# Optimization experiments

Measured on AMD Instinct MI355X. Metric: run time of the kernel, lower is better.

The kernel has to match this reference:

```python
import jax, jax.numpy as jnp
import numpy as np

DIM = 2048
H = 16
DH = DIM // H          # 128 per-head content dim
LATENT = 512
D_ROPE = 64
B, S = 2, 2048
ROPE_THETA = 10000.0


def _rope_cos_sin(seq_len, d_rope, dtype=jnp.float32):
    # [S, d_rope] cos/sin tables, rotate-half convention
    inv_freq = 1.0 / (ROPE_THETA ** (jnp.arange(0, d_rope, 2, dtype=jnp.float32) / d_rope))
    freqs = jnp.arange(seq_len, dtype=jnp.float32)[:, None] * inv_freq[None, :]  # [S, d_rope/2]
    emb = jnp.concatenate([freqs, freqs], axis=-1)  # [S, d_rope]
    return jnp.cos(emb).astype(dtype), jnp.sin(emb).astype(dtype)


def _rotate_half(x):
    x1, x2 = jnp.split(x, 2, axis=-1)
    return jnp.concatenate([-x2, x1], axis=-1)


def _apply_rope(x, cos, sin):
    # x: [..., S, ..., d_rope]; cos/sin broadcastable to x
    return x * cos + _rotate_half(x) * sin


def setup_inputs() -> dict:
    key = jax.random.key(0)
    ks = jax.random.split(key, 6)
    std = 0.02
    return {
        "x": jax.random.normal(ks[0], (B, S, DIM), jnp.float32),
        "Wq": jax.random.normal(ks[1], (DIM, H * (DH + D_ROPE)), jnp.float32) * std,
        "Wdkv": jax.random.normal(ks[2], (DIM, LATENT), jnp.float32) * std,
        "Wkr": jax.random.normal(ks[3], (DIM, D_ROPE), jnp.float32) * std,
        "Wukv": jax.random.normal(ks[4], (LATENT, H * 2 * DH), jnp.float32) * std,
        "Wo": jax.random.normal(ks[5], (H * DH, DIM), jnp.float32) * std,
    }


def reference(x, Wq, Wdkv, Wkr, Wukv, Wo):
    Bd, Sd, _ = x.shape
    # --- queries: per-head content + decoupled rope part ---
    q = (x @ Wq).reshape(Bd, Sd, H, DH + D_ROPE)
    q_nope, q_rope = q[..., :DH], q[..., DH:]            # [B,S,H,DH], [B,S,H,D_ROPE]
    # --- compressed latent KV ---
    c_kv = x @ Wdkv                                      # [B,S,LATENT]
    kv = (c_kv @ Wukv).reshape(Bd, Sd, H, 2 * DH)
    k_nope, v = kv[..., :DH], kv[..., DH:]               # [B,S,H,DH]
    # --- shared (head-agnostic) rotary key ---
    k_rope = x @ Wkr                                     # [B,S,D_ROPE]
    cos, sin = _rope_cos_sin(Sd, D_ROPE, x.dtype)
    q_rope = _apply_rope(q_rope, cos[None, :, None, :], sin[None, :, None, :])
    k_rope = _apply_rope(k_rope, cos[None, :, :], sin[None, :, :])
    # --- attention scores: content + decoupled rope term ---
    scale = 1.0 / jnp.sqrt(jnp.asarray(DH + D_ROPE, x.dtype))
    scores = jnp.einsum("bqhd,bkhd->bhqk", q_nope, k_nope)
    scores = scores + jnp.einsum("bqhd,bkd->bhqk", q_rope, k_rope)
    scores = scores * scale
    causal = jnp.tril(jnp.ones((Sd, Sd), dtype=bool))
    scores = jnp.where(causal[None, None, :, :], scores, jnp.asarray(-1e9, x.dtype))
    attn = jax.nn.softmax(scores, axis=-1)               # [B,H,S,S]
    out = jnp.einsum("bhqk,bkhd->bqhd", attn, v).reshape(Bd, Sd, H * DH)
    return out @ Wo                                      # [B,S,DIM]
```

## Files before the change

### kernel.cpp

```cpp
#include <hip/hip_runtime.h>
#include <hip/hip_bf16.h>

using bf16 = __hip_bfloat16;
typedef __bf16 bf16x8 __attribute__((ext_vector_type(8)));
typedef float f32x4 __attribute__((ext_vector_type(4)));

#define MFMA16(A, B, C) __builtin_amdgcn_mfma_f32_16x16x32_bf16((A), (B), (C), 0, 0, 0)

__device__ __forceinline__ void store_elem(bf16* p, float v) { *p = __float2bfloat16(v); }
__device__ __forceinline__ void store_elem(float* p, float v) { *p = v; }

__device__ __forceinline__ unsigned short f2bu(float x) {
    bf16 t = __float2bfloat16(x);
    return *(unsigned short*)&t;
}

__device__ __forceinline__ void async_cp16(const bf16* g, bf16* l) {
    __builtin_amdgcn_global_load_lds(
        (const __attribute__((address_space(1))) void*)g,
        (__attribute__((address_space(3))) void*)l, 16, 0, 0);
}

__global__ void cvt_fp32_bf16(const float* __restrict__ src, bf16* __restrict__ dst) {
    int i = (blockIdx.x * 256 + threadIdx.x) * 4;
    float4 v = *(const float4*)(src + i);
    bf16 o[4] = {__float2bfloat16(v.x), __float2bfloat16(v.y),
                 __float2bfloat16(v.z), __float2bfloat16(v.w)};
    *(uint2*)(dst + i) = *(const uint2*)o;
}

__global__ void wtrans(const float* __restrict__ src, bf16* __restrict__ dst,
                       int K, int N) {
    __shared__ bf16 t[32][33];
    int n0 = blockIdx.x * 32, k0 = blockIdx.y * 32;
    #pragma unroll
    for (int i = 0; i < 4; ++i) {
        int r = threadIdx.y + i * 8;
        t[r][threadIdx.x] = __float2bfloat16(src[(size_t)(k0 + r) * N + n0 + threadIdx.x]);
    }
    __syncthreads();
    #pragma unroll
    for (int i = 0; i < 4; ++i) {
        int r = threadIdx.y + i * 8;
        dst[(size_t)(n0 + r) * K + k0 + threadIdx.x] = t[threadIdx.x][r];
    }
}

__global__ void zerofill(bf16* __restrict__ p) {
    p[blockIdx.x * 256 + threadIdx.x] = __float2bfloat16(0.0f);
}

template <typename CT>
__global__ __launch_bounds__(256) void gemm_bt(
    const bf16* __restrict__ A, int lda,
    const bf16* __restrict__ Bt, int ldb,
    CT* __restrict__ C, int ldc, int K) {
    __shared__ bf16 As[2][128 * 32];
    __shared__ bf16 Bs[2][128 * 32];
    const int nwg = gridDim.x * gridDim.y;
    const int flat = blockIdx.y * gridDim.x + blockIdx.x;
    const int swz = (flat & 7) * (nwg >> 3) + (flat >> 3);
    const int m0 = (swz / gridDim.x) * 128;
    const int n0 = (swz % gridDim.x) * 128;
    const int tid = threadIdx.x;
    const int lane = tid & 63;
    const int wave = tid >> 6;
    const int wm = (wave >> 1) * 64;
    const int wn = (wave & 1) * 64;
    const int lr = lane & 15;
    const int lq = lane >> 4;
    const int sr = tid >> 2;
    const int sc = (tid & 3) * 8;
    const int wbase = wave * 512;

    f32x4 acc[4][4] = {};

#define G_STAGE(BUF, KO) do {                                                  \
        async_cp16(A + (size_t)(m0 + sr) * lda + (KO) + sc, As[BUF] + wbase);  \
        async_cp16(A + (size_t)(m0 + sr + 64) * lda + (KO) + sc,               \
                   As[BUF] + 2048 + wbase);                                    \
        async_cp16(Bt + (size_t)(n0 + sr) * ldb + (KO) + sc, Bs[BUF] + wbase); \
        async_cp16(Bt + (size_t)(n0 + sr + 64) * ldb + (KO) + sc,              \
                   Bs[BUF] + 2048 + wbase);                                    \
    } while (0)

    G_STAGE(0, 0);
    __syncthreads();
    int cur = 0;
    for (int k0 = 0; k0 < K; k0 += 32) {
        if (k0 + 32 < K) G_STAGE(cur ^ 1, k0 + 32);
        bf16x8 af[4], bfr[4];
        #pragma unroll
        for (int t = 0; t < 4; ++t) {
            af[t]  = *(const bf16x8*)(As[cur] + (wm + t * 16 + lr) * 32 + lq * 8);
            bfr[t] = *(const bf16x8*)(Bs[cur] + (wn + t * 16 + lr) * 32 + lq * 8);
        }
        #pragma unroll
        for (int mt = 0; mt < 4; ++mt)
            #pragma unroll
            for (int nt = 0; nt < 4; ++nt)
                acc[mt][nt] = MFMA16(af[mt], bfr[nt], acc[mt][nt]);
        __syncthreads();
        cur ^= 1;
    }
#undef G_STAGE
    #pragma unroll
    for (int mt = 0; mt < 4; ++mt)
        #pragma unroll
        for (int nt = 0; nt < 4; ++nt)
            #pragma unroll
            for (int r = 0; r < 4; ++r) {
                int row = m0 + wm + mt * 16 + lq * 4 + r;
                int col = n0 + wn + nt * 16 + lr;
                store_elem(C + (size_t)row * ldc + col, acc[mt][nt][r]);
            }
}

__global__ __launch_bounds__(256) void gemm_kv(
    const bf16* __restrict__ A, int lda,
    const bf16* __restrict__ Bt, int ldb,
    bf16* __restrict__ kbuf, bf16* __restrict__ vT, int K) {
    __shared__ bf16 As[2][128 * 32];
    __shared__ bf16 Bs[2][128 * 32];
    const int nwg = gridDim.x * gridDim.y;
    const int flat = blockIdx.y * gridDim.x + blockIdx.x;
    const int swz = (flat & 7) * (nwg >> 3) + (flat >> 3);
    const int m0 = (swz / gridDim.x) * 128;
    const int n0 = (swz % gridDim.x) * 128;
    const int tid = threadIdx.x;
    const int lane = tid & 63;
    const int wave = tid >> 6;
    const int wm = (wave >> 1) * 64;
    const int wn = (wave & 1) * 64;
    const int lr = lane & 15;
    const int lq = lane >> 4;
    const int sr = tid >> 2;
    const int sc = (tid & 3) * 8;
    const int wbase = wave * 512;

    f32x4 acc[4][4] = {};

#define G_STAGE(BUF, KO) do {                                                  \
        async_cp16(A + (size_t)(m0 + sr) * lda + (KO) + sc, As[BUF] + wbase);  \
        async_cp16(A + (size_t)(m0 + sr + 64) * lda + (KO) + sc,               \
                   As[BUF] + 2048 + wbase);                                    \
        async_cp16(Bt + (size_t)(n0 + sr) * ldb + (KO) + sc, Bs[BUF] + wbase); \
        async_cp16(Bt + (size_t)(n0 + sr + 64) * ldb + (KO) + sc,              \
                   Bs[BUF] + 2048 + wbase);                                    \
    } while (0)

    G_STAGE(0, 0);
    __syncthreads();
    int cur = 0;
    for (int k0 = 0; k0 < K; k0 += 32) {
        if (k0 + 32 < K) G_STAGE(cur ^ 1, k0 + 32);
        bf16x8 af[4], bfr[4];
        #pragma unroll
        for (int t = 0; t < 4; ++t) {
            af[t]  = *(const bf16x8*)(As[cur] + (wm + t * 16 + lr) * 32 + lq * 8);
            bfr[t] = *(const bf16x8*)(Bs[cur] + (wn + t * 16 + lr) * 32 + lq * 8);
        }
        #pragma unroll
        for (int mt = 0; mt < 4; ++mt)
            #pragma unroll
            for (int nt = 0; nt < 4; ++nt)
                acc[mt][nt] = MFMA16(af[mt], bfr[nt], acc[mt][nt]);
        __syncthreads();
        cur ^= 1;
    }
#undef G_STAGE
    #pragma unroll
    for (int mt = 0; mt < 4; ++mt)
        #pragma unroll
        for (int nt = 0; nt < 4; ++nt) {
            int colbase = n0 + wn + nt * 16;
            int h = colbase >> 8;
            int rr = (colbase & 255) + lr;
            #pragma unroll
            for (int r = 0; r < 4; ++r) {
                int row = m0 + wm + mt * 16 + lq * 4 + r;
                bf16 val = __float2bfloat16(acc[mt][nt][r]);
                if (rr < 128) {
                    kbuf[(size_t)row * 2048 + h * 128 + rr] = val;
                } else {
                    int dv = rr - 128;
                    int b = row >> 11, s = row & 2047;
                    vT[((size_t)((b * 16 + h) * 128 + dv)) * 2048 + s] = val;
                }
            }
        }
}

__global__ void rope_kernel(bf16* __restrict__ XW) {
    int v = blockIdx.x;
    int row = blockIdx.y * 4 + threadIdx.y;
    int i = threadIdx.x;
    int s = row & 2047;
    int cbase = (v < 16) ? v * 192 + 128 : 3072;
    size_t base = (size_t)row * 3712 + cbase;
    float xi = __bfloat162float(XW[base + i]);
    float xp = __shfl_xor(xi, 32);
    int j = i & 31;
    float inv = exp2f(-(float)j * (13.287712379549449f / 32.0f));
    float ang = (float)s * inv;
    float c = cosf(ang), sn = sinf(ang);
    float res = (i < 32) ? (xi * c - xp * sn) : (xi * c + xp * sn);
    XW[base + i] = __float2bfloat16(res);
}

__global__ __launch_bounds__(256, 2) void attn_kernel(
    const bf16* __restrict__ XW, const bf16* __restrict__ kbuf,
    const bf16* __restrict__ vT, bf16* __restrict__ attn_out,
    bf16* __restrict__ opart, float* __restrict__ mlbuf) {
    const int bid = blockIdx.x;
    const int half = bid >> 8;
    const int rem = bid & 255;
    const int bh = rem & 31;
    const int p = rem >> 5;
    const int b = bh >> 4, h = bh & 15;
    const int tid = threadIdx.x;
    const int wave = tid >> 6;
    const int lane = tid & 63;
    const int lr = lane & 15, lq = lane >> 4;

    __shared__ bf16 Ks[2][64 * 128];
    __shared__ bf16 Vs[128 * 64];
    __shared__ bf16 Pm[4 * 32 * 72];
    bf16* Pw = Pm + wave * (32 * 72);

    const bf16* xwb = XW + (size_t)b * 2048 * 3712;
    const bf16* kb  = kbuf + (size_t)b * 2048 * 2048 + h * 128;
    const bf16* rp  = xwb + 3072;
    const bf16* vTb = vT + (size_t)bh * 128 * 2048;

    const float sc2 = 0.07216878364870323f * 1.4426950408889634f;

    const int s_rsub = lane >> 4;
    const int s_j    = lane & 15;
#define STAGE_K(N0, BUF) do {                                                  \
        _Pragma("unroll")                                                      \
        for (int k_ = 0; k_ < 4; ++k_) {                                       \
            int i_ = wave * 4 + k_;                                            \
            int r_ = i_ * 4 + s_rsub;                                          \
            int j_ = s_j ^ (r_ & 7);                                           \
            async_cp16(kb + (size_t)((N0) + r_) * 2048 + j_ * 8,               \
                       (BUF) + i_ * 512);                                      \
        }                                                                      \
    } while (0)

#define STAGE_V(N0) do {                                                       \
        _Pragma("unroll")                                                      \
        for (int k_ = 0; k_ < 4; ++k_) {                                       \
            int i_ = wave * 4 + k_;                                            \
            int r_ = i_ * 8 + (lane >> 3);                                     \
            int j_ = (lane & 7) ^ (r_ & 7);                                    \
            async_cp16(vTb + (size_t)r_ * 2048 + (N0) + j_ * 8,                \
                       Vs + i_ * 512);                                         \
        }                                                                      \
    } while (0)

    const int rs = lr & 7;
    int koff[4];
    #pragma unroll
    for (int c = 0; c < 4; ++c) koff[c] = ((c * 4 + lq) ^ rs) * 8;
    int voff[2];
    voff[0] = (lq ^ rs) * 8;
    voff[1] = ((4 + lq) ^ rs) * 8;

    #pragma unroll 1
    for (int ph = 0; ph < 2; ++ph) {
        const int u = ph ? (15 - p) : p;
        const int qw = u * 128 + wave * 32;
        const int hnt = u + 1;
        const int t0 = half ? hnt : 0;
        const int t1 = half ? (2 * u + 2) : hnt;

        bf16x8 qf[2][6];
        #pragma unroll
        for (int nf = 0; nf < 2; ++nf) {
            size_t ro = (size_t)(qw + nf * 16 + lr) * 3712 + h * 192;
            #pragma unroll
            for (int c = 0; c < 6; ++c)
                qf[nf][c] = *(const bf16x8*)(xwb + ro + c * 32 + lq * 8);
        }

        f32x4 o[2][8] = {};
        float m_i[2], l_i[2];
        m_i[0] = m_i[1] = -1e30f;
        l_i[0] = l_i[1] = 0.0f;

        STAGE_K(t0 * 64, Ks[0]);
        int par = 0;

        for (int t = t0; t < t1; ++t) {
            const int n0 = t * 64;
            __syncthreads();

            bf16x8 rf[2][4];
            #pragma unroll
            for (int c = 0; c < 2; ++c)
                #pragma unroll
                for (int mt = 0; mt < 4; ++mt)
                    rf[c][mt] = *(const bf16x8*)(rp + (size_t)(n0 + mt * 16 + lr) * 3712 + c * 32 + lq * 8);

            STAGE_V(n0);
            if (t + 1 < t1) STAGE_K((t + 1) * 64, Ks[par ^ 1]);

            if (n0 < qw + 32) {
                const bf16* Kc = Ks[par];
                f32x4 st[4][2] = {};
                __builtin_amdgcn_s_setprio(1);
                #pragma unroll
                for (int c = 0; c < 4; ++c) {
                    #pragma unroll
                    for (int mt = 0; mt < 4; ++mt) {
                        bf16x8 kf = *(const bf16x8*)(Kc + (mt * 16 + lr) * 128 + koff[c]);
                        st[mt][0] = MFMA16(kf, qf[0][c], st[mt][0]);
                        st[mt][1] = MFMA16(kf, qf[1][c], st[mt][1]);
                    }
                }
                #pragma unroll
                for (int c = 0; c < 2; ++c) {
                    #pragma unroll
                    for (int mt = 0; mt < 4; ++mt) {
                        st[mt][0] = MFMA16(rf[c][mt], qf[0][c + 4], st[mt][0]);
                        st[mt][1] = MFMA16(rf[c][mt], qf[1][c + 4], st[mt][1]);
                    }
                }
                __builtin_amdgcn_s_setprio(0);

                #pragma unroll
                for (int nf = 0; nf < 2; ++nf) {
                    int q = qw + nf * 16 + lr;
                    f32x4 a[4];
                    #pragma unroll
                    for (int mt = 0; mt < 4; ++mt) a[mt] = st[mt][nf];
                    if (n0 + 63 > qw + nf * 16) {
                        #pragma unroll
                        for (int mt = 0; mt < 4; ++mt)
                            #pragma unroll
                            for (int r = 0; r < 4; ++r) {
                                int kid = n0 + mt * 16 + lq * 4 + r;
                                if (kid > q) a[mt][r] = -1e30f;
                            }
                    }
                    f32x4 m4 = a[0];
                    #pragma unroll
                    for (int mt = 1; mt < 4; ++mt)
                        #pragma unroll
                        for (int r = 0; r < 4; ++r) m4[r] = fmaxf(m4[r], a[mt][r]);
                    float vm = fmaxf(fmaxf(m4[0], m4[1]), fmaxf(m4[2], m4[3]));
                    vm = fmaxf(vm, __shfl_xor(vm, 16));
                    vm = fmaxf(vm, __shfl_xor(vm, 32));
                    vm *= sc2;
                    if (__any(vm > m_i[nf] + 8.0f)) {
                        float mnew = fmaxf(m_i[nf], vm);
                        float alpha = exp2f(m_i[nf] - mnew);
                        m_i[nf] = mnew;
                        l_i[nf] *= alpha;
                        #pragma unroll
                        for (int dt = 0; dt < 8; ++dt)
                            #pragma unroll
                            for (int r = 0; r < 4; ++r) o[nf][dt][r] *= alpha;
                    }
                    float mi = m_i[nf];
                    float ps = 0.0f;
                    #pragma unroll
                    for (int mt = 0; mt < 4; ++mt) {
                        unsigned short pk[4];
                        #pragma unroll
                        for (int r = 0; r < 4; ++r) {
                            float pv = exp2f(fmaf(a[mt][r], sc2, -mi));
                            ps += pv;
                            pk[r] = f2bu(pv);
                        }
                        *(uint2*)((unsigned short*)Pw + (nf * 16 + lr) * 72 + mt * 16 + lq * 4) =
                            *(uint2*)pk;
                    }
                    ps += __shfl_xor(ps, 16);
                    ps += __shfl_xor(ps, 32);
                    l_i[nf] += ps;
                }
            }

            __syncthreads();

            if (n0 < qw + 32) {
                bf16x8 ptf[2][2];
                #pragma unroll
                for (int nf = 0; nf < 2; ++nf)
                    #pragma unroll
                    for (int kt = 0; kt < 2; ++kt)
                        ptf[nf][kt] = *(const bf16x8*)(Pw + (nf * 16 + lr) * 72 + kt * 32 + lq * 8);
                __builtin_amdgcn_s_setprio(1);
                #pragma unroll
                for (int kt = 0; kt < 2; ++kt)
                    #pragma unroll
                    for (int dt = 0; dt < 8; ++dt) {
                        bf16x8 vfr = *(const bf16x8*)(Vs + (dt * 16 + lr) * 64 + voff[kt]);
                        o[0][dt] = MFMA16(vfr, ptf[0][kt], o[0][dt]);
                        o[1][dt] = MFMA16(vfr, ptf[1][kt], o[1][dt]);
                    }
                __builtin_amdgcn_s_setprio(0);
            }
            par ^= 1;
        }

        #pragma unroll
        for (int nf = 0; nf < 2; ++nf) {
            float l = l_i[nf];
            float wsc = (l > 0.0f) ? (1.0f / l) : 0.0f;
            float sst = (l > 0.0f) ? (m_i[nf] + log2f(l)) : -1e30f;
            __asm__ volatile("s_waitcnt lgkmcnt(0)" ::: "memory");
            #pragma unroll
            for (int dt = 0; dt < 8; ++dt) {
                unsigned short pk[4];
                #pragma unroll
                for (int r = 0; r < 4; ++r) pk[r] = f2bu(o[nf][dt][r] * wsc);
                *(uint2*)((unsigned short*)Pw + lr * 136 + dt * 16 + lq * 4) = *(uint2*)pk;
            }
            __asm__ volatile("s_waitcnt lgkmcnt(0)" ::: "memory");
            int ql = lane >> 2, cs = (lane & 3) * 32;
            int qrow = qw + nf * 16 + ql;
            uint4 d[4];
            #pragma unroll
            for (int k = 0; k < 4; ++k)
                d[k] = *(const uint4*)(Pw + ql * 136 + cs + k * 8);
            bf16* dst = (half ? opart : attn_out) +
                        (size_t)(b * 2048 + qrow) * 2048 + h * 128 + cs;
            #pragma unroll
            for (int k = 0; k < 4; ++k) *(uint4*)(dst + k * 8) = d[k];
            if (lane < 16) {
                int q2 = qw + nf * 16 + lane;
                mlbuf[((size_t)(b * 2048 + q2) * 16 + h) * 2 + half] = sst;
            }
        }
    }
#undef STAGE_K
#undef STAGE_V
}

__global__ void attn_merge(const bf16* __restrict__ opart,
                           const float* __restrict__ mlbuf,
                           bf16* __restrict__ attn_out) {
    int bs = blockIdx.x;
    int h = blockIdx.y * 2 + threadIdx.y;
    int tx = threadIdx.x;
    const float* mlp = mlbuf + ((size_t)bs * 16 + h) * 2;
    float s0 = mlp[0], s1 = mlp[1];
    size_t off = (size_t)bs * 2048 + h * 128 + tx;
    float o0 = __bfloat162float(attn_out[off]);
    float o1 = __bfloat162float(opart[off]);
    float m = fmaxf(s0, s1);
    float w0 = exp2f(s0 - m);
    float w1 = exp2f(s1 - m);
    float v = (o0 * w0 + o1 * w1) / (w0 + w1);
    attn_out[off] = __float2bfloat16(v);
}

extern "C" void kernel_launch(void* const* d_in, const int* in_sizes, int n_in,
                              void* d_out, int out_size, void* d_ws, size_t ws_size,
                              hipStream_t stream) {
    const float* x    = (const float*)d_in[0];
    const float* Wq   = (const float*)d_in[1];
    const float* Wdkv = (const float*)d_in[2];
    const float* Wkr  = (const float*)d_in[3];
    const float* Wukv = (const float*)d_in[4];
    const float* Wo   = (const float*)d_in[5];
    float* out = (float*)d_out;

    char* ws = (char*)d_ws;
    bf16* XW       = (bf16*)(ws);
    bf16* kbuf     = (bf16*)(ws + 30408704);
    bf16* vT       = (bf16*)(ws + 47185920);
    bf16* attn_out = (bf16*)(ws + 63963136);
    bf16* opart    = (bf16*)(ws + 80740352);
    float* mlbuf   = (float*)(ws + 97517568);
    bf16* xb       = (bf16*)(ws + 30408704);
    bf16* WcatT    = (bf16*)(ws + 47185920);
    bf16* WukvT    = (bf16*)(ws + 63963136);
    bf16* WoT      = (bf16*)(ws + 47185920);

    dim3 tb(32, 8);
    cvt_fp32_bf16<<<8192, 256, 0, stream>>>(x, xb);
    wtrans<<<dim3(96, 64), tb, 0, stream>>>(Wq, WcatT, 2048, 3072);
    wtrans<<<dim3(2, 64), tb, 0, stream>>>(Wkr, WcatT + (size_t)3072 * 2048, 2048, 64);
    wtrans<<<dim3(16, 64), tb, 0, stream>>>(Wdkv, WcatT + (size_t)3136 * 2048, 2048, 512);
    zerofill<<<512, 256, 0, stream>>>(WcatT + (size_t)3648 * 2048);
    wtrans<<<dim3(128, 16), tb, 0, stream>>>(Wukv, WukvT, 512, 4096);

    gemm_bt<bf16><<<dim3(29, 32), 256, 0, stream>>>(xb, 2048, WcatT, 2048, XW, 3712, 2048);
    rope_kernel<<<dim3(17, 1024), dim3(64, 4), 0, stream>>>(XW);
    gemm_kv<<<dim3(32, 32), 256, 0, stream>>>(XW + 3136, 3712, WukvT, 512, kbuf, vT, 512);
    attn_kernel<<<dim3(512), 256, 0, stream>>>(XW, kbuf, vT, attn_out, opart, mlbuf);
    attn_merge<<<dim3(4096, 8), dim3(128, 2), 0, stream>>>(opart, mlbuf, attn_out);
    wtrans<<<dim3(64, 64), tb, 0, stream>>>(Wo, WoT, 2048, 2048);
    gemm_bt<float><<<dim3(16, 32), 256, 0, stream>>>(attn_out, 2048, WoT, 2048, out, 2048, 2048);
}
```

Before: 457.5 us.

## Use 256x256 swizzled-LDS GEMM tiles and merge prep kernels into one launch

The projection GEMM and the KV up-projection GEMM move from 128x128 tiles with K-step 32 to 256x256 tiles with K-step 64. They run 8 waves per block and use XOR-swizzled LDS layouts to avoid bank conflicts. The padded columns beyond 3712 are zero-filled and masked on store. The input conversion, weight transposes and zero-fill are merged into one prep kernel, which cuts launch overhead. The larger tiles need 128KB of LDS per block, which limits occupancy to one block per CU and launches fewer blocks, so CUs may be less evenly loaded.

```diff
diff --git a/kernel.cpp b/kernel.cpp
--- a/kernel.cpp
+++ b/kernel.cpp
@@ -21,12 +21,52 @@
         (__attribute__((address_space(3))) void*)l, 16, 0, 0);
 }
 
-__global__ void cvt_fp32_bf16(const float* __restrict__ src, bf16* __restrict__ dst) {
-    int i = (blockIdx.x * 256 + threadIdx.x) * 4;
-    float4 v = *(const float4*)(src + i);
-    bf16 o[4] = {__float2bfloat16(v.x), __float2bfloat16(v.y),
-                 __float2bfloat16(v.z), __float2bfloat16(v.w)};
-    *(uint2*)(dst + i) = *(const uint2*)o;
+__device__ __forceinline__ void wtrans_body(
+    const float* __restrict__ src, bf16* __restrict__ dst, int K, int N,
+    int bx, int by, int tx, int ty, bf16 (*t)[33]) {
+    int n0 = bx * 32, k0 = by * 32;
+    #pragma unroll
+    for (int i = 0; i < 4; ++i) {
+        int r = ty + i * 8;
+        t[r][tx] = __float2bfloat16(src[(size_t)(k0 + r) * N + n0 + tx]);
+    }
+    __syncthreads();
+    #pragma unroll
+    for (int i = 0; i < 4; ++i) {
+        int r = ty + i * 8;
+        dst[(size_t)(n0 + r) * K + k0 + tx] = t[tx][r];
+    }
+}
+
+__global__ void prep(const float* __restrict__ x, bf16* __restrict__ xb,
+                     const float* __restrict__ Wq, const float* __restrict__ Wkr,
+                     const float* __restrict__ Wdkv, const float* __restrict__ Wukv,
+                     bf16* __restrict__ WcatT, bf16* __restrict__ WukvT) {
+    __shared__ bf16 tbuf[32][33];
+    int bid = blockIdx.x;
+    int tid = threadIdx.x;
+    int tx = tid & 31, ty = tid >> 5;
+    if (bid < 8192) {
+        int i = (bid * 256 + tid) * 4;
+        float4 v = *(const float4*)(x + i);
+        bf16 o[4] = {__float2bfloat16(v.x), __float2bfloat16(v.y),
+                     __float2bfloat16(v.z), __float2bfloat16(v.w)};
+        *(uint2*)(xb + i) = *(const uint2*)o;
+        return;
+    }
+    bid -= 8192;
+    if (bid < 6144) { wtrans_body(Wq, WcatT, 2048, 3072, bid % 96, bid / 96, tx, ty, tbuf); return; }
+    bid -= 6144;
+    if (bid < 128)  { wtrans_body(Wkr, WcatT + (size_t)3072 * 2048, 2048, 64, bid % 2, bid / 2, tx, ty, tbuf); return; }
+    bid -= 128;
+    if (bid < 1024) { wtrans_body(Wdkv, WcatT + (size_t)3136 * 2048, 2048, 512, bid % 16, bid / 16, tx, ty, tbuf); return; }
+    bid -= 1024;
+    if (bid < 1536) {
+        WcatT[(size_t)3648 * 2048 + bid * 256 + tid] = __float2bfloat16(0.0f);
+        return;
+    }
+    bid -= 1536;
+    wtrans_body(Wukv, WukvT, 512, 4096, bid % 128, bid / 128, tx, ty, tbuf);
 }
 
 __global__ void wtrans(const float* __restrict__ src, bf16* __restrict__ dst,
@@ -46,8 +86,174 @@
     }
 }
 
-__global__ void zerofill(bf16* __restrict__ p) {
-    p[blockIdx.x * 256 + threadIdx.x] = __float2bfloat16(0.0f);
+template <typename CT>
+__global__ __launch_bounds__(512, 2) void gemm256(
+    const bf16* __restrict__ A, int lda,
+    const bf16* __restrict__ Bt, int ldb,
+    CT* __restrict__ C, int ldc, int K, int Nmax) {
+    __shared__ bf16 smem[65536];
+    const int nwg = gridDim.x * gridDim.y;
+    const int flat = blockIdx.y * gridDim.x + blockIdx.x;
+    const int swz = (flat & 7) * (nwg >> 3) + (flat >> 3);
+    const int m0 = (swz / gridDim.x) * 256;
+    const int n0 = (swz % gridDim.x) * 256;
+    const int tid = threadIdx.x;
+    const int lane = tid & 63;
+    const int wave = tid >> 6;
+    const int wr = wave >> 2;
+    const int wc = wave & 3;
+    const int lr = lane & 15;
+    const int lq = lane >> 4;
+
+    f32x4 acc[8][4] = {};
+
+#define STG256(MATP, LD, ROWBASE, DSTBASE, K0) do {                            \
+        _Pragma("unroll")                                                      \
+        for (int i_ = 0; i_ < 4; ++i_) {                                       \
+            int ig_ = i_ * 8 + wave;                                           \
+            int r_ = ig_ * 8 + (lane >> 3);                                    \
+            int c_ = (lane & 7) ^ (r_ & 7);                                    \
+            async_cp16((MATP) + (size_t)((ROWBASE) + r_) * (LD) + (K0) + c_ * 8,\
+                       (DSTBASE) + ig_ * 512);                                 \
+        }                                                                      \
+    } while (0)
+
+    STG256(A, lda, m0, smem, 0);
+    STG256(Bt, ldb, n0, smem + 32768, 0);
+    __syncthreads();
+    int cur = 0;
+    const int nT = K >> 6;
+    for (int t = 0; t < nT; ++t) {
+        if (t + 1 < nT) {
+            STG256(A, lda, m0, smem + (cur ^ 1) * 16384, (t + 1) * 64);
+            STG256(Bt, ldb, n0, smem + 32768 + (cur ^ 1) * 16384, (t + 1) * 64);
+        }
+        const bf16* Ab = smem + cur * 16384;
+        const bf16* Bb = smem + 32768 + cur * 16384;
+        #pragma unroll
+        for (int kk = 0; kk < 2; ++kk) {
+            bf16x8 af[8], bfr[4];
+            #pragma unroll
+            for (int mt = 0; mt < 8; ++mt) {
+                int ra = wr * 128 + mt * 16 + lr;
+                af[mt] = *(const bf16x8*)(Ab + ra * 64 + ((kk * 4 + lq) ^ (ra & 7)) * 8);
+            }
+            #pragma unroll
+            for (int nt = 0; nt < 4; ++nt) {
+                int rb = wc * 64 + nt * 16 + lr;
+                bfr[nt] = *(const bf16x8*)(Bb + rb * 64 + ((kk * 4 + lq) ^ (rb & 7)) * 8);
+            }
+            #pragma unroll
+            for (int mt = 0; mt < 8; ++mt)
+                #pragma unroll
+                for (int nt = 0; nt < 4; ++nt)
+                    acc[mt][nt] = MFMA16(af[mt], bfr[nt], acc[mt][nt]);
+        }
+        __syncthreads();
+        cur ^= 1;
+    }
+#undef STG256
+    #pragma unroll
+    for (int mt = 0; mt < 8; ++mt)
+        #pragma unroll
+        for (int nt = 0; nt < 4; ++nt) {
+            int col = n0 + wc * 64 + nt * 16 + lr;
+            if (col < Nmax) {
+                #pragma unroll
+                for (int r = 0; r < 4; ++r) {
+                    int row = m0 + wr * 128 + mt * 16 + lq * 4 + r;
+                    store_elem(C + (size_t)row * ldc + col, acc[mt][nt][r]);
+                }
+            }
+        }
+}
+
+__global__ __launch_bounds__(512, 2) void gemm256_kv(
+    const bf16* __restrict__ A, int lda,
+    const bf16* __restrict__ Bt, int ldb,
+    bf16* __restrict__ kbuf, bf16* __restrict__ vT, int K) {
+    __shared__ bf16 smem[65536];
+    const int nwg = gridDim.x * gridDim.y;
+    const int flat = blockIdx.y * gridDim.x + blockIdx.x;
+    const int swz = (flat & 7) * (nwg >> 3) + (flat >> 3);
+    const int m0 = (swz / gridDim.x) * 256;
+    const int n0 = (swz % gridDim.x) * 256;
+    const int tid = threadIdx.x;
+    const int lane = tid & 63;
+    const int wave = tid >> 6;
+    const int wr = wave >> 2;
+    const int wc = wave & 3;
+    const int lr = lane & 15;
+    const int lq = lane >> 4;
+
+    f32x4 acc[8][4] = {};
+
+#define STG256(MATP, LD, ROWBASE, DSTBASE, K0) do {                            \
+        _Pragma("unroll")                                                      \
+        for (int i_ = 0; i_ < 4; ++i_) {                                       \
+            int ig_ = i_ * 8 + wave;                                           \
+            int r_ = ig_ * 8 + (lane >> 3);                                    \
+            int c_ = (lane & 7) ^ (r_ & 7);                                    \
+            async_cp16((MATP) + (size_t)((ROWBASE) + r_) * (LD) + (K0) + c_ * 8,\
+                       (DSTBASE) + ig_ * 512);                                 \
+        }                                                                      \
+    } while (0)
+
+    STG256(A, lda, m0, smem, 0);
+    STG256(Bt, ldb, n0, smem + 32768, 0);
+    __syncthreads();
+    int cur = 0;
+    const int nT = K >> 6;
+    for (int t = 0; t < nT; ++t) {
+        if (t + 1 < nT) {
+            STG256(A, lda, m0, smem + (cur ^ 1) * 16384, (t + 1) * 64);
+            STG256(Bt, ldb, n0, smem + 32768 + (cur ^ 1) * 16384, (t + 1) * 64);
+        }
+        const bf16* Ab = smem + cur * 16384;
+        const bf16* Bb = smem + 32768 + cur * 16384;
+        #pragma unroll
+        for (int kk = 0; kk < 2; ++kk) {
+            bf16x8 af[8], bfr[4];
+            #pragma unroll
+            for (int mt = 0; mt < 8; ++mt) {
+                int ra = wr * 128 + mt * 16 + lr;
+                af[mt] = *(const bf16x8*)(Ab + ra * 64 + ((kk * 4 + lq) ^ (ra & 7)) * 8);
+            }
+            #pragma unroll
+            for (int nt = 0; nt < 4; ++nt) {
+                int rb = wc * 64 + nt * 16 + lr;
+                bfr[nt] = *(const bf16x8*)(Bb + rb * 64 + ((kk * 4 + lq) ^ (rb & 7)) * 8);
+            }
+            #pragma unroll
+            for (int mt = 0; mt < 8; ++mt)
+                #pragma unroll
+                for (int nt = 0; nt < 4; ++nt)
+                    acc[mt][nt] = MFMA16(af[mt], bfr[nt], acc[mt][nt]);
+        }
+        __syncthreads();
+        cur ^= 1;
+    }
+#undef STG256
+    #pragma unroll
+    for (int mt = 0; mt < 8; ++mt)
+        #pragma unroll
+        for (int nt = 0; nt < 4; ++nt) {
+            int colbase = n0 + wc * 64 + nt * 16;
+            int h = colbase >> 8;
+            int rr = (colbase & 255) + lr;
+            #pragma unroll
+            for (int r = 0; r < 4; ++r) {
+                int row = m0 + wr * 128 + mt * 16 + lq * 4 + r;
+                bf16 val = __float2bfloat16(acc[mt][nt][r]);
+                if (rr < 128) {
+                    kbuf[(size_t)row * 2048 + h * 128 + rr] = val;
+                } else {
+                    int dv = rr - 128;
+                    int b = row >> 11, s = row & 2047;
+                    vT[((size_t)((b * 16 + h) * 128 + dv)) * 2048 + s] = val;
+                }
+            }
+        }
 }
 
 template <typename CT>
@@ -114,81 +320,6 @@
                 int col = n0 + wn + nt * 16 + lr;
                 store_elem(C + (size_t)row * ldc + col, acc[mt][nt][r]);
             }
-}
-
-__global__ __launch_bounds__(256) void gemm_kv(
-    const bf16* __restrict__ A, int lda,
-    const bf16* __restrict__ Bt, int ldb,
-    bf16* __restrict__ kbuf, bf16* __restrict__ vT, int K) {
-    __shared__ bf16 As[2][128 * 32];
-    __shared__ bf16 Bs[2][128 * 32];
-    const int nwg = gridDim.x * gridDim.y;
-    const int flat = blockIdx.y * gridDim.x + blockIdx.x;
-    const int swz = (flat & 7) * (nwg >> 3) + (flat >> 3);
-    const int m0 = (swz / gridDim.x) * 128;
-    const int n0 = (swz % gridDim.x) * 128;
-    const int tid = threadIdx.x;
-    const int lane = tid & 63;
-    const int wave = tid >> 6;
-    const int wm = (wave >> 1) * 64;
-    const int wn = (wave & 1) * 64;
-    const int lr = lane & 15;
-    const int lq = lane >> 4;
-    const int sr = tid >> 2;
-    const int sc = (tid & 3) * 8;
-    const int wbase = wave * 512;
-
-    f32x4 acc[4][4] = {};
-
-#define G_STAGE(BUF, KO) do {                                                  \
-        async_cp16(A + (size_t)(m0 + sr) * lda + (KO) + sc, As[BUF] + wbase);  \
-        async_cp16(A + (size_t)(m0 + sr + 64) * lda + (KO) + sc,               \
-                   As[BUF] + 2048 + wbase);                                    \
-        async_cp16(Bt + (size_t)(n0 + sr) * ldb + (KO) + sc, Bs[BUF] + wbase); \
-        async_cp16(Bt + (size_t)(n0 + sr + 64) * ldb + (KO) + sc,              \
-                   Bs[BUF] + 2048 + wbase);                                    \
-    } while (0)
-
-    G_STAGE(0, 0);
-    __syncthreads();
-    int cur = 0;
-    for (int k0 = 0; k0 < K; k0 += 32) {
-        if (k0 + 32 < K) G_STAGE(cur ^ 1, k0 + 32);
-        bf16x8 af[4], bfr[4];
-        #pragma unroll
-        for (int t = 0; t < 4; ++t) {
-            af[t]  = *(const bf16x8*)(As[cur] + (wm + t * 16 + lr) * 32 + lq * 8);
-            bfr[t] = *(const bf16x8*)(Bs[cur] + (wn + t * 16 + lr) * 32 + lq * 8);
-        }
-        #pragma unroll
-        for (int mt = 0; mt < 4; ++mt)
-            #pragma unroll
-            for (int nt = 0; nt < 4; ++nt)
-                acc[mt][nt] = MFMA16(af[mt], bfr[nt], acc[mt][nt]);
-        __syncthreads();
-        cur ^= 1;
-    }
-#undef G_STAGE
-    #pragma unroll
-    for (int mt = 0; mt < 4; ++mt)
-        #pragma unroll
-        for (int nt = 0; nt < 4; ++nt) {
-            int colbase = n0 + wn + nt * 16;
-            int h = colbase >> 8;
-            int rr = (colbase & 255) + lr;
-            #pragma unroll
-            for (int r = 0; r < 4; ++r) {
-                int row = m0 + wm + mt * 16 + lq * 4 + r;
-                bf16 val = __float2bfloat16(acc[mt][nt][r]);
-                if (rr < 128) {
-                    kbuf[(size_t)row * 2048 + h * 128 + rr] = val;
-                } else {
-                    int dv = rr - 128;
-                    int b = row >> 11, s = row & 2047;
-                    vT[((size_t)((b * 16 + h) * 128 + dv)) * 2048 + s] = val;
-                }
-            }
-        }
 }
 
 __global__ void rope_kernel(bf16* __restrict__ XW) {
@@ -481,19 +612,16 @@
     bf16* WukvT    = (bf16*)(ws + 63963136);
     bf16* WoT      = (bf16*)(ws + 47185920);
 
-    dim3 tb(32, 8);
-    cvt_fp32_bf16<<<8192, 256, 0, stream>>>(x, xb);
-    wtrans<<<dim3(96, 64), tb, 0, stream>>>(Wq, WcatT, 2048, 3072);
-    wtrans<<<dim3(2, 64), tb, 0, stream>>>(Wkr, WcatT + (size_t)3072 * 2048, 2048, 64);
-    wtrans<<<dim3(16, 64), tb, 0, stream>>>(Wdkv, WcatT + (size_t)3136 * 2048, 2048, 512);
-    zerofill<<<512, 256, 0, stream>>>(WcatT + (size_t)3648 * 2048);
-    wtrans<<<dim3(128, 16), tb, 0, stream>>>(Wukv, WukvT, 512, 4096);
-
-    gemm_bt<bf16><<<dim3(29, 32), 256, 0, stream>>>(xb, 2048, WcatT, 2048, XW, 3712, 2048);
+    prep<<<19072, 256, 0, stream>>>(x, xb, Wq, Wkr, Wdkv, Wukv, WcatT, WukvT);
+
+    gemm256<bf16><<<dim3(15, 16), 512, 0, stream>>>(xb, 2048, WcatT, 2048,
+                                                    XW, 3712, 2048, 3712);
     rope_kernel<<<dim3(17, 1024), dim3(64, 4), 0, stream>>>(XW);
-    gemm_kv<<<dim3(32, 32), 256, 0, stream>>>(XW + 3136, 3712, WukvT, 512, kbuf, vT, 512);
+    gemm256_kv<<<dim3(16, 16), 512, 0, stream>>>(XW + 3136, 3712, WukvT, 512,
+                                                 kbuf, vT, 512);
     attn_kernel<<<dim3(512), 256, 0, stream>>>(XW, kbuf, vT, attn_out, opart, mlbuf);
+    wtrans<<<dim3(64, 64), dim3(32, 8), 0, stream>>>(Wo, WoT, 2048, 2048);
     attn_merge<<<dim3(4096, 8), dim3(128, 2), 0, stream>>>(opart, mlbuf, attn_out);
-    wtrans<<<dim3(64, 64), tb, 0, stream>>>(Wo, WoT, 2048, 2048);
-    gemm_bt<float><<<dim3(16, 32), 256, 0, stream>>>(attn_out, 2048, WoT, 2048, out, 2048, 2048);
-}
+    gemm_bt<float><<<dim3(16, 32), 256, 0, stream>>>(attn_out, 2048, WoT, 2048,
+                                                     out, 2048, 2048);
+}
```

Measured after the change: 381.3 us. 1.2x faster.
